# Optimization experiments

Measured on AMD Instinct MI355X. Metric: run time of the kernel, lower is better.

Reference implementation:

```python
import jax, jax.numpy as jnp
import numpy as np

N = 8388608
HID = 8
P = 10.0
EPS = 1e-8
LR = 1.0
EXP_P = float(np.exp(np.float32(P)))  # exp(10) ~ 22026.466


def setup_inputs() -> dict:
    key = jax.random.key(0)
    ks = jax.random.split(key, 12)
    s = 0.3
    inp = {
        "h": jnp.zeros((N, HID), jnp.float32),
        "g": jax.random.normal(ks[0], (N,), jnp.float32),
        # GRUCell params (flax: input denses no bias, hidden denses with bias)
        "Wi_r": jax.random.normal(ks[1], (2, HID), jnp.float32) * s,
        "Wh_r": jax.random.normal(ks[2], (HID, HID), jnp.float32) * s,
        "bh_r": jax.random.normal(ks[3], (HID,), jnp.float32) * s,
        "Wi_z": jax.random.normal(ks[4], (2, HID), jnp.float32) * s,
        "Wh_z": jax.random.normal(ks[5], (HID, HID), jnp.float32) * s,
        "bh_z": jax.random.normal(ks[6], (HID,), jnp.float32) * s,
        "Wi_n": jax.random.normal(ks[7], (2, HID), jnp.float32) * s,
        "Wh_n": jax.random.normal(ks[8], (HID, HID), jnp.float32) * s,
        "bh_n": jax.random.normal(ks[9], (HID,), jnp.float32) * s,
        # MLP: single Dense(1) (mlp_dims=(), trailing relu popped)
        "Wm": jax.random.normal(ks[10], (HID, 1), jnp.float32) * s,
        "bm": jax.random.normal(ks[11], (1,), jnp.float32) * s,
    }
    return inp


def reference(h, g, Wi_r, Wh_r, bh_r, Wi_z, Wh_z, bh_z, Wi_n, Wh_n, bh_n, Wm, bm):
    g2 = jax.lax.stop_gradient(g[..., None])            # [N,1]
    g_sign = jnp.sign(g2)
    g_log = jnp.log(jnp.abs(g2) + EPS) / P              # [N,1]
    g_in1 = jnp.concatenate([g_log, g_sign], axis=-1)   # [N,2]
    g_in2 = jnp.concatenate([-jnp.ones_like(g2), EXP_P * g2], axis=-1)
    g_in = jnp.where(g_log >= -1.0, g_in1, g_in2)       # [N,2] (broadcast select)

    # flax GRUCell: r,z gates sigmoid, candidate tanh, input dense has no bias
    r = jax.nn.sigmoid(g_in @ Wi_r + h @ Wh_r + bh_r)
    z = jax.nn.sigmoid(g_in @ Wi_z + h @ Wh_z + bh_z)
    n = jnp.tanh(g_in @ Wi_n + r * (h @ Wh_n + bh_n))
    h_new = (1.0 - z) * n + z * h                        # [N,8]

    outs = h_new @ Wm + bm                               # [N,1]
    out = -LR * jnp.exp(outs) * g2                       # [N,1]
    return h_new, out[..., 0]
```

## Files before the change

kernel.cpp:

```cpp
#include <hip/hip_runtime.h>


typedef float f32x2 __attribute__((ext_vector_type(2)));

#define PIN(x) asm volatile("" : "+v"(x))

#define QP(x, ctrl) __int_as_float(__builtin_amdgcn_mov_dpp(__float_as_int(x), (ctrl), 0xF, 0xF, false))
#define QP_B0 0x00
#define QP_B1 0x55
#define QP_B2 0xAA
#define QP_B3 0xFF
#define QP_X1 0xB1
#define QP_X2 0x4E

#define PK_FMA_BLO(d, a, bp) \
    asm("v_pk_fma_f32 %0, %1, %2, %0 op_sel:[0,0,0] op_sel_hi:[1,0,1]" \
        : "+v"(d) : "v"(a), "v"(bp))
#define PK_FMA_BHI(d, a, bp) \
    asm("v_pk_fma_f32 %0, %1, %2, %0 op_sel:[0,1,0] op_sel_hi:[1,1,1]" \
        : "+v"(d) : "v"(a), "v"(bp))
#define PK_FMA3_BLO(d, a, bp, c) \
    asm("v_pk_fma_f32 %0, %1, %2, %3 op_sel:[0,0,0] op_sel_hi:[1,0,1]" \
        : "=v"(d) : "v"(a), "v"(bp), "v"(c))
#define PK_MUL_BLO(d, a, bp) \
    asm("v_pk_mul_f32 %0, %1, %2 op_sel:[0,0] op_sel_hi:[1,0]" \
        : "=v"(d) : "v"(a), "v"(bp))

__global__ __launch_bounds__(256, 4) void gru_l2l_kernel(
    const float* __restrict__ hp, const float* __restrict__ gp,
    const float* __restrict__ Wi_r, const float* __restrict__ Wh_r, const float* __restrict__ bh_r,
    const float* __restrict__ Wi_z, const float* __restrict__ Wh_z, const float* __restrict__ bh_z,
    const float* __restrict__ Wi_n, const float* __restrict__ Wh_n, const float* __restrict__ bh_n,
    const float* __restrict__ Wm, const float* __restrict__ bm,
    float* __restrict__ out, int nrows)
{
    const int npairs = nrows << 2;
    const int tid    = blockIdx.x * blockDim.x + threadIdx.x;
    const int stride = blockDim.x * gridDim.x;
    const int m      = tid & 3;
    const int c0     = m << 1;

    const float L2E = 1.44269504088896341f;

    f32x2 wir0 = { Wi_r[c0] * L2E,     Wi_r[c0 + 1] * L2E };
    f32x2 wir1 = { Wi_r[8 + c0] * L2E, Wi_r[8 + c0 + 1] * L2E };
    f32x2 wiz0 = { Wi_z[c0] * L2E,     Wi_z[c0 + 1] * L2E };
    f32x2 wiz1 = { Wi_z[8 + c0] * L2E, Wi_z[8 + c0 + 1] * L2E };
    f32x2 win0 = { Wi_n[c0],           Wi_n[c0 + 1] };
    f32x2 win1 = { Wi_n[8 + c0],       Wi_n[8 + c0 + 1] };
    f32x2 whr[8], whz[8], whn[8];
#pragma unroll
    for (int k = 0; k < 8; ++k) {
        whr[k] = (f32x2){ Wh_r[k * 8 + c0] * L2E, Wh_r[k * 8 + c0 + 1] * L2E };
        whz[k] = (f32x2){ Wh_z[k * 8 + c0] * L2E, Wh_z[k * 8 + c0 + 1] * L2E };
        whn[k] = (f32x2){ Wh_n[k * 8 + c0],       Wh_n[k * 8 + c0 + 1] };
    }
    f32x2 br = { bh_r[c0] * L2E, bh_r[c0 + 1] * L2E };
    f32x2 bz = { bh_z[c0] * L2E, bh_z[c0 + 1] * L2E };
    f32x2 bn = { bh_n[c0],       bh_n[c0 + 1] };
    float wmx  = Wm[c0], wmy = Wm[c0 + 1];
    float bmv2 = bm[0] * L2E;

    PIN(wir0); PIN(wir1); PIN(wiz0); PIN(wiz1); PIN(win0); PIN(win1);
#pragma unroll
    for (int k = 0; k < 8; ++k) { PIN(whr[k]); PIN(whz[k]); PIN(whn[k]); }
    PIN(br); PIN(bz); PIN(bn); PIN(wmx); PIN(wmy); PIN(bmv2);
    asm volatile("" ::: "memory");

    const f32x2* __restrict__ hp2  = (const f32x2*)hp;
    f32x2* __restrict__       out2 = (f32x2*)out;
    float* __restrict__       outo = out + ((long)nrows << 3);

    auto body = [&](const f32x2 hv, const float g, const int p) -> float {
        const float ag = fabsf(g) + 1e-8f;
        const float lg = __builtin_amdgcn_logf(ag) * 0.069314718055994531f;
        const bool  hi = (lg >= -1.0f);
        f32x2 gin;
        gin.x = hi ? lg : -1.0f;
        gin.y = hi ? ((g > 0.0f) ? 1.0f : -1.0f)
                   : 22026.465794806718f * g;

        f32x2 hb0, hb1, hb2, hb3;
        hb0.x = QP(hv.x, QP_B0); hb0.y = QP(hv.y, QP_B0);
        hb1.x = QP(hv.x, QP_B1); hb1.y = QP(hv.y, QP_B1);
        hb2.x = QP(hv.x, QP_B2); hb2.y = QP(hv.y, QP_B2);
        hb3.x = QP(hv.x, QP_B3); hb3.y = QP(hv.y, QP_B3);

        f32x2 ar, az, an, hn;
        PK_FMA3_BLO(ar, wir0, gin, br);
        PK_FMA_BHI (ar, wir1, gin);
        PK_FMA3_BLO(az, wiz0, gin, bz);
        PK_FMA_BHI (az, wiz1, gin);
        PK_MUL_BLO (an, win0, gin);
        PK_FMA_BHI (an, win1, gin);
        PK_FMA3_BLO(hn, whn[0], hb0, bn);
        PK_FMA_BLO (ar, whr[0], hb0);
        PK_FMA_BLO (az, whz[0], hb0);
        PK_FMA_BHI (ar, whr[1], hb0);
        PK_FMA_BHI (az, whz[1], hb0);
        PK_FMA_BHI (hn, whn[1], hb0);
#define DOT2(Q, K0, K1) \
        PK_FMA_BLO(ar, whr[K0], hb##Q); \
        PK_FMA_BLO(az, whz[K0], hb##Q); \
        PK_FMA_BLO(hn, whn[K0], hb##Q); \
        PK_FMA_BHI(ar, whr[K1], hb##Q); \
        PK_FMA_BHI(az, whz[K1], hb##Q); \
        PK_FMA_BHI(hn, whn[K1], hb##Q);
        DOT2(1, 2, 3) DOT2(2, 4, 5) DOT2(3, 6, 7)
#undef DOT2

        const float rx = __builtin_amdgcn_rcpf(1.0f + __builtin_amdgcn_exp2f(-ar.x));
        const float ry = __builtin_amdgcn_rcpf(1.0f + __builtin_amdgcn_exp2f(-ar.y));
        const float zx = __builtin_amdgcn_rcpf(1.0f + __builtin_amdgcn_exp2f(-az.x));
        const float zy = __builtin_amdgcn_rcpf(1.0f + __builtin_amdgcn_exp2f(-az.y));

        const float prex = fmaf(rx, hn.x, an.x);
        const float prey = fmaf(ry, hn.y, an.y);
        const float tx = __builtin_amdgcn_exp2f(-2.885390081777927f * fabsf(prex));
        const float ty = __builtin_amdgcn_exp2f(-2.885390081777927f * fabsf(prey));
        const float nx = copysignf((1.0f - tx) * __builtin_amdgcn_rcpf(1.0f + tx), prex);
        const float ny = copysignf((1.0f - ty) * __builtin_amdgcn_rcpf(1.0f + ty), prey);
        const float hnx = fmaf(zx, hv.x - nx, nx);
        const float hny = fmaf(zy, hv.y - ny, ny);
        f32x2 ho; ho.x = hnx; ho.y = hny;
        out2[p] = ho;

        float s = fmaf(hny, wmy, hnx * wmx);
        s += QP(s, QP_X1);
        s += QP(s, QP_X2);
        return s;
    };

    const int stride2 = stride << 1;
    int p = tid;
    for (; p + stride < npairs; p += stride2) {
        const int pB = p + stride;
        const f32x2 hvA = hp2[p];
        const float gA  = gp[p >> 2];
        const f32x2 hvB = hp2[pB];
        const float gB  = gp[pB >> 2];

        const float sA = body(hvA, gA, p);
        const float sB = body(hvB, gB, pB);

        if (m == 0) {
            outo[p >> 2]  = -__builtin_amdgcn_exp2f(fmaf(sA, L2E, bmv2)) * gA;
            outo[pB >> 2] = -__builtin_amdgcn_exp2f(fmaf(sB, L2E, bmv2)) * gB;
        }
    }
    if (p < npairs) {
        const f32x2 hv = hp2[p];
        const float g  = gp[p >> 2];
        const float s  = body(hv, g, p);
        if (m == 0) {
            outo[p >> 2] = -__builtin_amdgcn_exp2f(fmaf(s, L2E, bmv2)) * g;
        }
    }
}

extern "C" void kernel_launch(void* const* d_in, const int* in_sizes, int n_in,
                              void* d_out, int out_size, void* d_ws, size_t ws_size,
                              hipStream_t stream) {
    const float* hp   = (const float*)d_in[0];
    const float* gp   = (const float*)d_in[1];
    const float* Wi_r = (const float*)d_in[2];
    const float* Wh_r = (const float*)d_in[3];
    const float* bh_r = (const float*)d_in[4];
    const float* Wi_z = (const float*)d_in[5];
    const float* Wh_z = (const float*)d_in[6];
    const float* bh_z = (const float*)d_in[7];
    const float* Wi_n = (const float*)d_in[8];
    const float* Wh_n = (const float*)d_in[9];
    const float* bh_n = (const float*)d_in[10];
    const float* Wm   = (const float*)d_in[11];
    const float* bm   = (const float*)d_in[12];
    const int nrows   = in_sizes[1];

    gru_l2l_kernel<<<8192, 256, 0, stream>>>(hp, gp, Wi_r, Wh_r, bh_r,
                                             Wi_z, Wh_z, bh_z,
                                             Wi_n, Wh_n, bh_n,
                                             Wm, bm, (float*)d_out, nrows);
}
```

Baseline: 558.3 us.

## Software-pipeline grid-stride loop loads and relax launch bounds occupancy

Measured after the change: 560.8 us. About the same (+0.4%).

```diff
diff --git a/kernel.cpp b/kernel.cpp
--- a/kernel.cpp
+++ b/kernel.cpp
@@ -26,7 +26,7 @@
     asm("v_pk_mul_f32 %0, %1, %2 op_sel:[0,0] op_sel_hi:[1,0]" \
         : "=v"(d) : "v"(a), "v"(bp))
 
-__global__ __launch_bounds__(256, 4) void gru_l2l_kernel(
+__global__ __launch_bounds__(256, 2) void gru_l2l_kernel(
     const float* __restrict__ hp, const float* __restrict__ gp,
     const float* __restrict__ Wi_r, const float* __restrict__ Wh_r, const float* __restrict__ bh_r,
     const float* __restrict__ Wi_z, const float* __restrict__ Wh_z, const float* __restrict__ bh_z,
@@ -131,29 +131,41 @@
         return s;
     };
 
+    auto finish = [&](const float s, const float g, const int p) {
+        const float ov = -__builtin_amdgcn_exp2f(fmaf(s, L2E, bmv2)) * g;
+        if (m == 0) outo[p >> 2] = ov;
+    };
+
     const int stride2 = stride << 1;
-    int p = tid;
-    for (; p + stride < npairs; p += stride2) {
-        const int pB = p + stride;
-        const f32x2 hvA = hp2[p];
-        const float gA  = gp[p >> 2];
-        const f32x2 hvB = hp2[pB];
-        const float gB  = gp[pB >> 2];
+    int pA = tid;
+    if (pA < npairs) {
+        int pB = pA + stride;
+        const bool hasB = (pB < npairs);
+        f32x2 hvA = hp2[pA];
+        float gA  = gp[pA >> 2];
+        f32x2 hvB = hvA;
+        float gB  = gA;
+        if (hasB) { hvB = hp2[pB]; gB = gp[pB >> 2]; }
 
-        const float sA = body(hvA, gA, p);
-        const float sB = body(hvB, gB, pB);
+        int pA2 = pA + stride2, pB2 = pB + stride2;
+        while (pB2 < npairs) {
+            f32x2 hvA2 = hp2[pA2]; float gA2 = gp[pA2 >> 2];
+            f32x2 hvB2 = hp2[pB2]; float gB2 = gp[pB2 >> 2];
 
-        if (m == 0) {
-            outo[p >> 2]  = -__builtin_amdgcn_exp2f(fmaf(sA, L2E, bmv2)) * gA;
-            outo[pB >> 2] = -__builtin_amdgcn_exp2f(fmaf(sB, L2E, bmv2)) * gB;
+            finish(body(hvA, gA, pA), gA, pA);
+            finish(body(hvB, gB, pB), gB, pB);
+
+            pA = pA2; pB = pB2;
+            hvA = hvA2; gA = gA2;
+            hvB = hvB2; gB = gB2;
+            pA2 += stride2; pB2 += stride2;
         }
-    }
-    if (p < npairs) {
-        const f32x2 hv = hp2[p];
-        const float g  = gp[p >> 2];
-        const float s  = body(hv, g, p);
-        if (m == 0) {
-            outo[p >> 2] = -__builtin_amdgcn_exp2f(fmaf(s, L2E, bmv2)) * g;
+        finish(body(hvA, gA, pA), gA, pA);
+        if (pB < npairs) finish(body(hvB, gB, pB), gB, pB);
+        if (pA2 < npairs) {
+            const f32x2 hv = hp2[pA2];
+            const float g  = gp[pA2 >> 2];
+            finish(body(hv, g, pA2), g, pA2);
         }
     }
 }
```
